# Optimization experiments

Measured on AMD Instinct MI355X. Metric: run time of the kernel, lower is better.

## Reference

```python
import jax, jax.numpy as jnp
import numpy as np

DIM = 1024
H = 16
DH = DIM // H  # 64


def _l2norm(a):
    # matches torch F.normalize(dim=-1, eps=1e-12)
    n = jnp.linalg.norm(a, axis=-1, keepdims=True)
    return a / jnp.maximum(n, 1e-12)


def setup_inputs() -> dict:
    key = jax.random.key(0)
    ks = jax.random.split(key, 6)
    B, T = 4, 4096
    s = 0.02
    return {
        "x": jax.random.normal(ks[0], (B, T, DIM), jnp.float32),
        "Wqkv": jax.random.normal(ks[1], (3 * DIM, DIM), jnp.float32) * s,
        "Wg": jax.random.normal(ks[2], (H, DIM), jnp.float32) * s,
        "bg": jnp.zeros((H,), jnp.float32),
        "Wb": jax.random.normal(ks[3], (H, DIM), jnp.float32) * s,
        "bb": jnp.zeros((H,), jnp.float32),
        "Wout": jax.random.normal(ks[4], (DIM, DIM), jnp.float32) * s,
    }


def reference(x, Wqkv, Wg, bg, Wb, bb, Wout):
    B, T, D = x.shape
    qkv = (x @ Wqkv.T).reshape(B, T, 3, H, DH)
    q = _l2norm(qkv[:, :, 0])   # [B,T,H,Dh]
    k = _l2norm(qkv[:, :, 1])
    v = qkv[:, :, 2]
    alpha = jax.nn.sigmoid(x @ Wg.T + bg)  # [B,T,H]
    beta = jax.nn.sigmoid(x @ Wb.T + bb)   # [B,T,H]

    # time-major for scan
    qT = jnp.moveaxis(q, 1, 0)  # [T,B,H,Dh]
    kT = jnp.moveaxis(k, 1, 0)
    vT = jnp.moveaxis(v, 1, 0)
    aT = jnp.moveaxis(alpha, 1, 0)  # [T,B,H]
    bT = jnp.moveaxis(beta, 1, 0)

    S0 = jnp.zeros((B, H, DH, DH), jnp.float32)

    def step(S, inp):
        q_t, k_t, v_t, a_t, b_t = inp
        Sk = jnp.einsum('bhij,bhj->bhi', S, k_t)          # S @ k_t
        a = a_t[..., None, None]
        b = b_t[..., None, None]
        # S = a * (S - b * (S k) k^T) + b * v k^T
        S = a * (S - b * Sk[..., :, None] * k_t[..., None, :]) \
            + b * v_t[..., :, None] * k_t[..., None, :]
        o = jnp.einsum('bhij,bhj->bhi', S, q_t)
        return S, o

    _, outs = jax.lax.scan(step, S0, (qT, kT, vT, aT, bT))  # [T,B,H,Dh]
    out = jnp.moveaxis(outs, 0, 1).reshape(B, T, D)
    return out @ Wout.T
```

## Files before the change

### kernel.cpp

```cpp
#include <hip/hip_runtime.h>
#include <hip/hip_bf16.h>

#define NB   4
#define NT   4096
#define BT   16384
#define NDIM 1024
#define NH   16
#define NDH  64
#define CC   64
#define NCH  (NT / CC)
#define NPAIR 64
#define NU   (NPAIR * NCH)
#define DBS  24

using u16 = unsigned short;
typedef __bf16 bf16x8 __attribute__((ext_vector_type(8)));
typedef float f32x4 __attribute__((ext_vector_type(4)));
typedef unsigned short u16x8 __attribute__((ext_vector_type(8)));
typedef unsigned short u16x4 __attribute__((ext_vector_type(4)));

__device__ __forceinline__ float bf2f(u16 b) { return __uint_as_float(((unsigned)b) << 16); }
__device__ __forceinline__ u16 f2bf(float f) {
  return __builtin_bit_cast(u16, __float2bfloat16(f));
}
__device__ __forceinline__ int swz(int row, int e) { return e ^ ((row & 7) << 3); }
__device__ __forceinline__ bf16x8 zfrag() {
  u16x8 z = {0, 0, 0, 0, 0, 0, 0, 0};
  return __builtin_bit_cast(bf16x8, z);
}

__global__ __launch_bounds__(256) void k_f32_to_bf16(const float* __restrict__ in,
                                                     u16* __restrict__ out, long n4) {
  long i = (long)blockIdx.x * blockDim.x + threadIdx.x;
  if (i >= n4) return;
  float4 f = reinterpret_cast<const float4*>(in)[i];
  u16x4 o;
  o.x = f2bf(f.x); o.y = f2bf(f.y); o.z = f2bf(f.z); o.w = f2bf(f.w);
  reinterpret_cast<u16x4*>(out)[i] = o;
}

__global__ __launch_bounds__(256) void k_build_wgb(const float* __restrict__ Wg,
                                                   const float* __restrict__ Wb,
                                                   u16* __restrict__ out) {
  int i = blockIdx.x * 256 + threadIdx.x;
  int row = i >> 10, col = i & 1023;
  float f = 0.f;
  if (row < 16)       f = Wg[row * 1024 + col];
  else if (row < 32)  f = Wb[(row - 16) * 1024 + col];
  out[i] = f2bf(f);
}

typedef unsigned int u32_as1 __attribute__((address_space(1)));
typedef unsigned int u32_as3 __attribute__((address_space(3)));
__device__ __forceinline__ void gload_lds16(const void* g, void* l) {
  __builtin_amdgcn_global_load_lds((const u32_as1*)g, (u32_as3*)l, 16, 0, 0);
}

template <typename OutT>
__global__ __launch_bounds__(256) void k_gemm_bt(const u16* __restrict__ A,
                                                 const u16* __restrict__ B,
                                                 OutT* __restrict__ C,
                                                 int M, int N, int K) {
  constexpr int BM = 128, BN = 128, BK = 32;
  __shared__ __align__(16) u16 As[BM * BK];
  __shared__ __align__(16) u16 Bs[BN * BK];
  const int tid = threadIdx.x;
  const int l = tid & 63, w = tid >> 6;
  const int tn = blockIdx.x, tm = blockIdx.y;
  const long a0 = (long)tm * BM * K;
  const long b0 = (long)tn * BN * K;
  const int srow = tid >> 2;
  const int scol = (tid & 3) << 3;
  const int wrow = (w >> 1) << 6;
  const int wcol = (w & 1) << 6;
  const int fr = l & 15, fq = l >> 4;

  f32x4 acc[4][4];
#pragma unroll
  for (int m = 0; m < 4; ++m)
#pragma unroll
    for (int n = 0; n < 4; ++n) acc[m][n] = f32x4{0.f, 0.f, 0.f, 0.f};

  for (int kk = 0; kk < K; kk += BK) {
    __syncthreads();
    const u16* gA = A + a0 + (long)srow * K + kk + scol;
    const u16* gB = B + b0 + (long)srow * K + kk + scol;
    gload_lds16(gA,                &As[(w * 16) * BK]);
    gload_lds16(gA + 64 * (long)K, &As[(64 + w * 16) * BK]);
    gload_lds16(gB,                &Bs[(w * 16) * BK]);
    gload_lds16(gB + 64 * (long)K, &Bs[(64 + w * 16) * BK]);
    __syncthreads();

    bf16x8 af[4], bfv[4];
#pragma unroll
    for (int m = 0; m < 4; ++m)
      af[m] = *(const bf16x8*)&As[(wrow + m * 16 + fr) * BK + (fq << 3)];
#pragma unroll
    for (int n = 0; n < 4; ++n)
      bfv[n] = *(const bf16x8*)&Bs[(wcol + n * 16 + fr) * BK + (fq << 3)];
#pragma unroll
    for (int m = 0; m < 4; ++m)
#pragma unroll
      for (int n = 0; n < 4; ++n)
        acc[m][n] = __builtin_amdgcn_mfma_f32_16x16x32_bf16(af[m], bfv[n], acc[m][n], 0, 0, 0);
  }

#pragma unroll
  for (int m = 0; m < 4; ++m) {
#pragma unroll
    for (int n = 0; n < 4; ++n) {
      const int r0 = tm * BM + wrow + m * 16 + fq * 4;
      const int c  = tn * BN + wcol + n * 16 + fr;
#pragma unroll
      for (int r = 0; r < 4; ++r) {
        float v = acc[m][n][r];
        long idx = (long)(r0 + r) * N + c;
        if constexpr (sizeof(OutT) == 2) C[idx] = f2bf(v);
        else                             C[idx] = v;
      }
    }
  }
}

template <typename OutT>
__global__ __launch_bounds__(512, 2) void k_gemm256(const u16* __restrict__ A,
                                                    const u16* __restrict__ B,
                                                    OutT* __restrict__ C,
                                                    int M, int N, int K) {
  __shared__ __align__(16) u16 As[2][2][256 * 32];
  __shared__ __align__(16) u16 Bs[2][2][256 * 32];
  const int tid = threadIdx.x;
  const int l = tid & 63, w = tid >> 6;
  const int wm = w >> 2, wn = w & 3;
  const int fr = l & 15, fq = l >> 4;
  const int nwg = gridDim.x;
  const int cpx = nwg >> 3;
  const int bid = blockIdx.x;
  const int sbid = (bid & 7) * cpx + (bid >> 3);
  const int ntn = N >> 8;
  const int tm = sbid / ntn, tn = sbid - tm * ntn;
  const long a0 = (long)tm * 256 * K;
  const long b0 = (long)tn * 256 * K;
  const int srow0 = tid >> 2;
  const int scol8 = (((tid & 3) ^ ((tid >> 4) & 3)) << 3);
  const int cswz = ((fq ^ ((fr >> 2) & 3)) << 3);
  const int NKT = K >> 6;

  auto stage_half = [&](int kt, int buf, int hf) {
    const int ks = hf >> 1;
    const u16* Gp = (hf & 1) ? B : A;
    const long g0 = ((hf & 1) ? b0 : a0) + (long)kt * 64 + ks * 32 + scol8;
    u16* lb = (hf & 1) ? &Bs[buf][ks][w * 512] : &As[buf][ks][w * 512];
#pragma unroll
    for (int r = 0; r < 2; ++r)
      gload_lds16(Gp + g0 + (long)(r * 128 + srow0) * K, lb + r * 4096);
  };

  f32x4 acc[8][4];
#pragma unroll
  for (int m = 0; m < 8; ++m)
#pragma unroll
    for (int n = 0; n < 4; ++n) acc[m][n] = f32x4{0.f, 0.f, 0.f, 0.f};

  stage_half(0, 0, 0); stage_half(0, 0, 1); stage_half(0, 0, 2); stage_half(0, 0, 3);

  for (int kt = 0; kt < NKT; ++kt) {
    const int bi = kt & 1;
    const bool pf = (kt + 1 < NKT);
    asm volatile("s_waitcnt vmcnt(4)" ::: "memory");
    __builtin_amdgcn_sched_barrier(0);
    __builtin_amdgcn_s_barrier();
    __builtin_amdgcn_sched_barrier(0);
    {
      const u16* ap = &As[bi][0][(wm * 128 + fr) * 32 + cswz];
      const u16* bp = &Bs[bi][0][(wn * 64 + fr) * 32 + cswz];
      bf16x8 bfr[4], afr[4];
#pragma unroll
      for (int n = 0; n < 4; ++n) bfr[n] = *(const bf16x8*)(bp + n * 512);
#pragma unroll
      for (int m = 0; m < 4; ++m) afr[m] = *(const bf16x8*)(ap + m * 512);
      if (pf) stage_half(kt + 1, bi ^ 1, 0);
      __builtin_amdgcn_s_setprio(1);
#pragma unroll
      for (int m = 0; m < 4; ++m)
#pragma unroll
        for (int n = 0; n < 4; ++n)
          acc[m][n] = __builtin_amdgcn_mfma_f32_16x16x32_bf16(afr[m], bfr[n], acc[m][n], 0, 0, 0);
      __builtin_amdgcn_s_setprio(0);
#pragma unroll
      for (int m = 0; m < 4; ++m) afr[m] = *(const bf16x8*)(ap + (4 + m) * 512);
      if (pf) stage_half(kt + 1, bi ^ 1, 1);
      __builtin_amdgcn_s_setprio(1);
#pragma unroll
      for (int m = 0; m < 4; ++m)
#pragma unroll
        for (int n = 0; n < 4; ++n)
          acc[4 + m][n] = __builtin_amdgcn_mfma_f32_16x16x32_bf16(afr[m], bfr[n], acc[4 + m][n], 0, 0, 0);
      __builtin_amdgcn_s_setprio(0);
    }
    if (pf) { asm volatile("s_waitcnt vmcnt(4)" ::: "memory"); }
    else    { asm volatile("s_waitcnt vmcnt(0)" ::: "memory"); }
    __builtin_amdgcn_sched_barrier(0);
    __builtin_amdgcn_s_barrier();
    __builtin_amdgcn_sched_barrier(0);
    {
      const u16* ap = &As[bi][1][(wm * 128 + fr) * 32 + cswz];
      const u16* bp = &Bs[bi][1][(wn * 64 + fr) * 32 + cswz];
      bf16x8 bfr[4], afr[4];
#pragma unroll
      for (int n = 0; n < 4; ++n) bfr[n] = *(const bf16x8*)(bp + n * 512);
#pragma unroll
      for (int m = 0; m < 4; ++m) afr[m] = *(const bf16x8*)(ap + m * 512);
      if (pf) stage_half(kt + 1, bi ^ 1, 2);
      __builtin_amdgcn_s_setprio(1);
#pragma unroll
      for (int m = 0; m < 4; ++m)
#pragma unroll
        for (int n = 0; n < 4; ++n)
          acc[m][n] = __builtin_amdgcn_mfma_f32_16x16x32_bf16(afr[m], bfr[n], acc[m][n], 0, 0, 0);
      __builtin_amdgcn_s_setprio(0);
#pragma unroll
      for (int m = 0; m < 4; ++m) afr[m] = *(const bf16x8*)(ap + (4 + m) * 512);
      if (pf) stage_half(kt + 1, bi ^ 1, 3);
      __builtin_amdgcn_s_setprio(1);
#pragma unroll
      for (int m = 0; m < 4; ++m)
#pragma unroll
        for (int n = 0; n < 4; ++n)
          acc[4 + m][n] = __builtin_amdgcn_mfma_f32_16x16x32_bf16(afr[m], bfr[n], acc[4 + m][n], 0, 0, 0);
      __builtin_amdgcn_s_setprio(0);
    }
  }

#pragma unroll
  for (int m = 0; m < 8; ++m)
#pragma unroll
    for (int n = 0; n < 4; ++n) {
      const int row0 = tm * 256 + wm * 128 + m * 16 + fq * 4;
      const int col  = tn * 256 + wn * 64 + n * 16 + fr;
#pragma unroll
      for (int r = 0; r < 4; ++r) {
        long idx = (long)(row0 + r) * N + col;
        if constexpr (sizeof(OutT) == 2) C[idx] = f2bf(acc[m][n][r]);
        else                             C[idx] = acc[m][n][r];
      }
    }
}

__global__ __launch_bounds__(256) void k_gates_fin(const float* __restrict__ raw,
                                                   const float* __restrict__ bg,
                                                   const float* __restrict__ bb,
                                                   float* __restrict__ alpha,
                                                   float* __restrict__ beta) {
  int i = blockIdx.x * 256 + threadIdx.x;
  if (i >= BT * NH) return;
  int bt = i >> 4, h = i & 15;
  float ga = raw[(long)bt * 128 + h] + bg[h];
  float gb = raw[(long)bt * 128 + 16 + h] + bb[h];
  alpha[i] = 1.f / (1.f + __expf(-ga));
  beta[i]  = 1.f / (1.f + __expf(-gb));
}

__global__ __launch_bounds__(256, 3) void k_prep(u16* __restrict__ qkv,
                                                 const float* __restrict__ alpha,
                                                 const float* __restrict__ beta,
                                                 float* __restrict__ A63G,
                                                 u16* __restrict__ ob) {
  __shared__ __align__(16) u16 Ks[64 * 64];
  __shared__ __align__(16) u16 WTs[128 * 64];
  __shared__ __align__(16) u16 Lb[64 * 64];
  __shared__ __align__(16) u16 MqS[64 * 64];
  __shared__ __align__(16) u16 KdT[64 * 64];
  __shared__ __align__(16) u16 Db[4 * 16 * DBS];
  __shared__ float cvec[64], Avec[64], bvec[64], nkinv[64], nqinv[64];

  const int unit = blockIdx.x;
  const int pair = unit >> 6, ch = unit & 63;
  const int b = pair >> 4, h = pair & 15;
  const int tid = threadIdx.x, l = tid & 63, w = tid >> 6;
  const int fr = l & 15, fq = l >> 4;
  const long t0 = (long)b * NT + (long)ch * CC;

  u16x8 kreg[2], vreg[2], qreg[2];
  int srow_[2], sseg_[2];
#pragma unroll
  for (int p = 0; p < 2; ++p) {
    int idx = p * 256 + tid;
    srow_[p] = idx >> 3; sseg_[p] = (idx & 7) * 8;
    long g = (t0 + srow_[p]) * 3072 + h * 64 + sseg_[p];
    qreg[p] = *(const u16x8*)&qkv[g];
    kreg[p] = *(const u16x8*)&qkv[g + 1024];
    vreg[p] = *(const u16x8*)&qkv[g + 2048];
  }
  const int ar = w * 16 + fr;
  u16x8 qa[2];
#pragma unroll
  for (int kk = 0; kk < 2; ++kk)
    qa[kk] = *(const u16x8*)&qkv[(t0 + ar) * 3072 + h * 64 + kk * 32 + fq * 8];

  if (tid < 64) { nkinv[tid] = 0.f; nqinv[tid] = 0.f; }
  if (w == 0) {
    float av = alpha[(t0 + l) * 16 + h];
    float bv = beta[(t0 + l) * 16 + h];
    float cl = __log2f(av);
#pragma unroll
    for (int d = 1; d < 64; d <<= 1) {
      float up = __shfl_up(cl, d);
      if (l >= d) cl += up;
    }
    float A = exp2f(cl);
    cvec[l] = cl; Avec[l] = A; bvec[l] = bv;
    if (l == 63) A63G[unit] = A;
  }
  __syncthreads();

#pragma unroll
  for (int p = 0; p < 2; ++p) {
    int row = srow_[p], seg = sseg_[p];
    *(u16x8*)&Ks[row * 64 + swz(row, seg)] = kreg[p];
    float kss = 0.f, qss = 0.f;
    const float bs = bvec[row];
#pragma unroll
    for (int e = 0; e < 8; ++e) {
      float kf = bf2f(kreg[p][e]), qf = bf2f(qreg[p][e]);
      kss += kf * kf; qss += qf * qf;
      int c = seg + e;
      WTs[c * 64 + swz(c, row)] = f2bf(bs * bf2f(vreg[p][e]));
    }
    atomicAdd(&nkinv[row], kss);
    atomicAdd(&nqinv[row], qss);
  }
  __syncthreads();

  if (tid < 64)       nkinv[tid] = rsqrtf(fmaxf(nkinv[tid], 1e-24f));
  else if (tid < 128) nqinv[tid - 64] = rsqrtf(fmaxf(nqinv[tid - 64], 1e-24f));
  __syncthreads();

  f32x4 akk[4], aqk[4];
#pragma unroll
  for (int n = 0; n < 4; ++n) { akk[n] = f32x4{0, 0, 0, 0}; aqk[n] = f32x4{0, 0, 0, 0}; }
  {
    bf16x8 afK[2], afQ[2];
#pragma unroll
    for (int kk = 0; kk < 2; ++kk) {
      afK[kk] = __builtin_bit_cast(bf16x8, *(const u16x8*)&Ks[ar * 64 + swz(ar, kk * 32 + fq * 8)]);
      afQ[kk] = __builtin_bit_cast(bf16x8, qa[kk]);
    }
#pragma unroll
    for (int n = 0; n < 4; ++n) {
      const int br = n * 16 + fr;
#pragma unroll
      for (int kk = 0; kk < 2; ++kk) {
        bf16x8 bk = __builtin_bit_cast(bf16x8, *(const u16x8*)&Ks[br * 64 + swz(br, kk * 32 + fq * 8)]);
        akk[n] = __builtin_amdgcn_mfma_f32_16x16x32_bf16(afK[kk], bk, akk[n], 0, 0, 0);
        aqk[n] = __builtin_amdgcn_mfma_f32_16x16x32_bf16(afQ[kk], bk, aqk[n], 0, 0, 0);
      }
    }
  }
  {
    const int j = tid & 63, tg4 = tid >> 6;
    const float c63 = cvec[63];
    u16 kb[16], kd[16];
#pragma unroll
    for (int tt = 0; tt < 16; ++tt) {
      int t = tg4 * 16 + tt;
      float kv = bf2f(Ks[t * 64 + swz(t, j)]) * nkinv[t];
      kb[tt] = f2bf(bvec[t] * Avec[t] * kv);
      kd[tt] = f2bf(exp2f(c63 - cvec[t]) * kv);
    }
#pragma unroll
    for (int g8 = 0; g8 < 2; ++g8) {
      u16x8 o1, o2;
#pragma unroll
      for (int e = 0; e < 8; ++e) { o1[e] = kb[g8 * 8 + e]; o2[e] = kd[g8 * 8 + e]; }
      int colg = tg4 * 16 + g8 * 8;
      *(u16x8*)&WTs[(64 + j) * 64 + swz(64 + j, colg)] = o1;
      *(u16x8*)&KdT[j * 64 + swz(j, colg)] = o2;
    }
  }
#pragma unroll
  for (int n = 0; n < 4; ++n)
#pragma unroll
    for (int r = 0; r < 4; ++r) {
      const int t = w * 16 + fq * 4 + r;
      const int s = n * 16 + fr;
      const float e = exp2f(cvec[t] - cvec[s]);
      Lb[t * 64 + swz(t, s)] = (s < t) ? f2bf(bvec[t] * e * nkinv[t] * nkinv[s] * akk[n][r]) : (u16)0;
      MqS[t * 64 + swz(t, s)] = (s <= t) ? f2bf(e * nqinv[t] * nkinv[s] * aqk[n][r]) : (u16)0;
    }
  __syncthreads();

  if (w == 0) {
    const int bi = l >> 4, c = l & 15;
    const int rb = bi * 16;
    float x[16];
#pragma unroll
    for (int u = 0; u < 16; ++u) {
      float a2 = (u == c) ? 1.f : 0.f;
#pragma unroll
      for (int s = 0; s < u; ++s)
        a2 -= bf2f(Lb[(rb + u) * 64 + swz(rb + u, rb + s)]) * x[s];
      x[u] = a2;
    }
#pragma unroll
    for (int u = 0; u < 16; ++u)
      Db[bi * 16 * DBS + u * DBS + c] = f2bf(x[u]);
  }
  __syncthreads();

  float ltil[6];
  {
    const int pbi[6] = {1, 2, 2, 3, 3, 3}, pbj[6] = {0, 0, 1, 0, 1, 2};
    const int tt = tid >> 4, s = tid & 15;
#pragma unroll
    for (int e = 0; e < 6; ++e) {
      int bi = pbi[e], bj = pbj[e];
      float a2 = 0.f;
#pragma unroll
      for (int u = 0; u < 16; ++u)
        a2 += bf2f(Db[bi * 16 * DBS + tt * DBS + u]) *
              bf2f(Lb[(bi * 16 + u) * 64 + swz(bi * 16 + u, bj * 16 + s)]);
      ltil[e] = a2;
    }
  }
  f32x4 rtacc[2][4];
#pragma unroll
  for (int rt2 = 0; rt2 < 2; ++rt2) {
    const int rrow = (w * 2 + rt2) * 16 + fr;
#pragma unroll
    for (int bi = 0; bi < 4; ++bi) {
      bf16x8 a2 = (fq < 2)
        ? __builtin_bit_cast(bf16x8, *(const u16x8*)&WTs[rrow * 64 + swz(rrow, bi * 16 + fq * 8)])
        : zfrag();
      bf16x8 b2 = (fq < 2)
        ? __builtin_bit_cast(bf16x8, *(const u16x8*)&Db[bi * 16 * DBS + fr * DBS + fq * 8])
        : zfrag();
      rtacc[rt2][bi] = __builtin_amdgcn_mfma_f32_16x16x32_bf16(a2, b2, f32x4{0, 0, 0, 0}, 0, 0, 0);
    }
  }
  __syncthreads();
  {
    const int pbi[6] = {1, 2, 2, 3, 3, 3}, pbj[6] = {0, 0, 1, 0, 1, 2};
    const int tt = tid >> 4, s = tid & 15;
#pragma unroll
    for (int e = 0; e < 6; ++e)
      Lb[(pbi[e] * 16 + tt) * 64 + swz(pbi[e] * 16 + tt, pbj[e] * 16 + s)] = f2bf(-ltil[e]);
  }
#pragma unroll
  for (int rt2 = 0; rt2 < 2; ++rt2)
#pragma unroll
    for (int bi = 0; bi < 4; ++bi)
#pragma unroll
      for (int r = 0; r < 4; ++r) {
        int rr = (w * 2 + rt2) * 16 + fq * 4 + r;
        WTs[rr * 64 + swz(rr, bi * 16 + fr)] = f2bf(rtacc[rt2][bi][r]);
      }
  __syncthreads();

#pragma unroll
  for (int rt2 = 0; rt2 < 2; ++rt2) {
    const int rrow = (w * 2 + rt2) * 16 + fr;
    const int wr0 = (w * 2 + rt2) * 16 + fq * 4;
#pragma unroll
    for (int i = 1; i < 4; ++i) {
      f32x4 a2;
#pragma unroll
      for (int r = 0; r < 4; ++r)
        a2[r] = bf2f(WTs[(wr0 + r) * 64 + swz(wr0 + r, i * 16 + fr)]);
      {
        bf16x8 af = __builtin_bit_cast(bf16x8, *(const u16x8*)&WTs[rrow * 64 + swz(rrow, fq * 8)]);
        bf16x8 bf_;
        if (i == 1) bf_ = (fq < 2)
          ? __builtin_bit_cast(bf16x8, *(const u16x8*)&Lb[(16 + fr) * 64 + swz(16 + fr, fq * 8)])
          : zfrag();
        else bf_ = __builtin_bit_cast(bf16x8, *(const u16x8*)&Lb[(i * 16 + fr) * 64 + swz(i * 16 + fr, fq * 8)]);
        a2 = __builtin_amdgcn_mfma_f32_16x16x32_bf16(af, bf_, a2, 0, 0, 0);
      }
      if (i == 3) {
        bf16x8 af = __builtin_bit_cast(bf16x8, *(const u16x8*)&WTs[rrow * 64 + swz(rrow, 32 + fq * 8)]);
        bf16x8 bf_ = (fq < 2)
          ? __builtin_bit_cast(bf16x8, *(const u16x8*)&Lb[(48 + fr) * 64 + swz(48 + fr, 32 + fq * 8)])
          : zfrag();
        a2 = __builtin_amdgcn_mfma_f32_16x16x32_bf16(af, bf_, a2, 0, 0, 0);
      }
#pragma unroll
      for (int r = 0; r < 4; ++r)
        WTs[(wr0 + r) * 64 + swz(wr0 + r, i * 16 + fr)] = f2bf(a2[r]);
    }
  }
  __syncthreads();

  u16 qpre[4][4];
#pragma unroll
  for (int n = 0; n < 4; ++n)
#pragma unroll
    for (int r = 0; r < 4; ++r)
      qpre[n][r] = qkv[(t0 + w * 16 + fq * 4 + r) * 3072 + h * 64 + n * 16 + fr];

  f32x4 aG[4], aU[4], aQe[4], aOi[4];
#pragma unroll
  for (int n = 0; n < 4; ++n) {
    aG[n] = f32x4{0, 0, 0, 0}; aU[n] = f32x4{0, 0, 0, 0};
    aQe[n] = f32x4{0, 0, 0, 0}; aOi[n] = f32x4{0, 0, 0, 0};
  }
  {
    bf16x8 aKd[2], aWv[2], aMq[2];
#pragma unroll
    for (int kk = 0; kk < 2; ++kk) {
      aKd[kk] = __builtin_bit_cast(bf16x8, *(const u16x8*)&KdT[ar * 64 + swz(ar, kk * 32 + fq * 8)]);
      aWv[kk] = __builtin_bit_cast(bf16x8, *(const u16x8*)&WTs[ar * 64 + swz(ar, kk * 32 + fq * 8)]);
      aMq[kk] = __builtin_bit_cast(bf16x8, *(const u16x8*)&MqS[ar * 64 + swz(ar, kk * 32 + fq * 8)]);
    }
#pragma unroll
    for (int n = 0; n < 4; ++n) {
      const int br = n * 16 + fr;
#pragma unroll
      for (int kk = 0; kk < 2; ++kk) {
        bf16x8 bTw = __builtin_bit_cast(bf16x8, *(const u16x8*)&WTs[(64 + br) * 64 + swz(64 + br, kk * 32 + fq * 8)]);
        bf16x8 bKd = __builtin_bit_cast(bf16x8, *(const u16x8*)&KdT[br * 64 + swz(br, kk * 32 + fq * 8)]);
        bf16x8 bWv = __builtin_bit_cast(bf16x8, *(const u16x8*)&WTs[br * 64 + swz(br, kk * 32 + fq * 8)]);
        aG[n]  = __builtin_amdgcn_mfma_f32_16x16x32_bf16(aKd[kk], bTw, aG[n], 0, 0, 0);
        aU[n]  = __builtin_amdgcn_mfma_f32_16x16x32_bf16(aWv[kk], bKd, aU[n], 0, 0, 0);
        aQe[n] = __builtin_amdgcn_mfma_f32_16x16x32_bf16(aMq[kk], bTw, aQe[n], 0, 0, 0);
        aOi[n] = __builtin_amdgcn_mfma_f32_16x16x32_bf16(aMq[kk], bWv, aOi[n], 0, 0, 0);
      }
    }
  }
  asm volatile("s_waitcnt vmcnt(0)" ::: "memory");
  __builtin_amdgcn_sched_barrier(0);
#pragma unroll
  for (int n = 0; n < 4; ++n)
#pragma unroll
    for (int r = 0; r < 4; ++r) {
      const int i = w * 16 + fq * 4 + r;
      const int cn = n * 16 + fr;
      const long grow = (t0 + i) * 3072 + h * 64 + swz(i, cn);
      qkv[grow]        = f2bf(Avec[i] * nqinv[i] * bf2f(qpre[n][r]) - aQe[n][r]);
      qkv[grow + 1024] = f2bf(-aG[n][r]);
      qkv[grow + 2048] = f2bf(aU[n][r]);
      ob[(t0 + i) * 1024 + h * 64 + cn] = f2bf(aOi[n][r]);
    }
}

__global__ __launch_bounds__(256) void k_seq(const u16* __restrict__ qkv,
                                             const float* __restrict__ A63G,
                                             u16* __restrict__ ob) {
  __shared__ __align__(16) u16 Sb[64 * 64];
  __shared__ __align__(16) u16 stg[2][4][64 * 64];
  __shared__ float a63s[64];
  const int pair = blockIdx.x;
  const int b = pair >> 4, h = pair & 15;
  const int tid = threadIdx.x, l = tid & 63, w = tid >> 6;
  const int fr = l & 15, fq = l >> 4;
  const int ar = w * 16 + fr;

  auto stage = [&](int c, int bi) {
    const long tg = (long)b * NT + (long)c * CC;
#pragma unroll
    for (int m = 0; m < 4; ++m)
#pragma unroll
      for (int p = 0; p < 2; ++p) {
        int idx = p * 256 + tid;
        int row = idx >> 3, seg = (idx & 7) * 8;
        const u16* src = (m < 3)
          ? &qkv[(tg + row) * 3072 + m * 1024 + h * 64 + seg]
          : &ob[(tg + row) * 1024 + h * 64 + seg];
        gload_lds16(src, &stg[bi][m][p * 2048 + w * 512]);
      }
  };

  if (tid < 64) a63s[tid] = A63G[pair * 64 + tid];
  for (int i = tid; i < 4096; i += 256) Sb[i] = 0;
  stage(0, 0);
  f32x4 sacc[4];
#pragma unroll
  for (int n = 0; n < 4; ++n) sacc[n] = f32x4{0, 0, 0, 0};
  asm volatile("s_waitcnt lgkmcnt(0)" ::: "memory");
  __builtin_amdgcn_sched_barrier(0);

  for (int c = 0; c < NCH; ++c) {
    const int bi = c & 1;
    const long tg = (long)b * NT + (long)c * CC;
    if (c + 1 < NCH) {
      stage(c + 1, bi ^ 1);
      asm volatile("s_waitcnt vmcnt(8)" ::: "memory");
    } else {
      asm volatile("s_waitcnt vmcnt(0)" ::: "memory");
    }
    __builtin_amdgcn_sched_barrier(0);
    __builtin_amdgcn_s_barrier();
    __builtin_amdgcn_sched_barrier(0);

    const u16* Qe = stg[bi][0];
    const u16* Gm = stg[bi][1];
    const u16* Um = stg[bi][2];
    const u16* Obl = stg[bi][3];

    bf16x8 aq[2];
#pragma unroll
    for (int kk = 0; kk < 2; ++kk)
      aq[kk] = __builtin_bit_cast(bf16x8, *(const u16x8*)&Qe[ar * 64 + swz(ar, kk * 32 + fq * 8)]);
    f32x4 ao[4];
#pragma unroll
    for (int n = 0; n < 4; ++n) ao[n] = f32x4{0, 0, 0, 0};
#pragma unroll
    for (int n = 0; n < 4; ++n) {
      const int br = n * 16 + fr;
#pragma unroll
      for (int kk = 0; kk < 2; ++kk) {
        bf16x8 sb = __builtin_bit_cast(bf16x8, *(const u16x8*)&Sb[br * 64 + swz(br, kk * 32 + fq * 8)]);
        ao[n] = __builtin_amdgcn_mfma_f32_16x16x32_bf16(aq[kk], sb, ao[n], 0, 0, 0);
      }
    }
    bf16x8 as_[2];
#pragma unroll
    for (int kk = 0; kk < 2; ++kk)
      as_[kk] = __builtin_bit_cast(bf16x8, *(const u16x8*)&Sb[ar * 64 + swz(ar, kk * 32 + fq * 8)]);
    const float A63 = a63s[c];
#pragma unroll
    for (int n = 0; n < 4; ++n) {
#pragma unroll
      for (int r = 0; r < 4; ++r) sacc[n][r] *= A63;
      const int br = n * 16 + fr;
#pragma unroll
      for (int kk = 0; kk < 2; ++kk) {
        bf16x8 g = __builtin_bit_cast(bf16x8, *(const u16x8*)&Gm[br * 64 + swz(br, kk * 32 + fq * 8)]);
        sacc[n] = __builtin_amdgcn_mfma_f32_16x16x32_bf16(as_[kk], g, sacc[n], 0, 0, 0);
      }
    }
#pragma unroll
    for (int n = 0; n < 4; ++n)
#pragma unroll
      for (int r = 0; r < 4; ++r) {
        const int i = w * 16 + fq * 4 + r;
        const int cn = n * 16 + fr;
        sacc[n][r] += bf2f(Um[i * 64 + swz(i, cn)]);
        float o = bf2f(Obl[i * 64 + cn]) + ao[n][r];
        ob[(tg + i) * 1024 + h * 64 + cn] = f2bf(o);
      }
    __builtin_amdgcn_s_barrier();
#pragma unroll
    for (int n = 0; n < 4; ++n)
#pragma unroll
      for (int r = 0; r < 4; ++r) {
        const int d = w * 16 + fq * 4 + r, j = n * 16 + fr;
        Sb[d * 64 + swz(d, j)] = f2bf(sacc[n][r]);
      }
    asm volatile("s_waitcnt lgkmcnt(0)" ::: "memory");
    __builtin_amdgcn_sched_barrier(0);
  }
}

extern "C" void kernel_launch(void* const* d_in, const int* in_sizes, int n_in,
                              void* d_out, int out_size, void* d_ws, size_t ws_size,
                              hipStream_t stream) {
  const float* x    = (const float*)d_in[0];
  const float* Wqkv = (const float*)d_in[1];
  const float* Wg   = (const float*)d_in[2];
  const float* bg   = (const float*)d_in[3];
  const float* Wb   = (const float*)d_in[4];
  const float* bb   = (const float*)d_in[5];
  const float* Wout = (const float*)d_in[6];
  float* out = (float*)d_out;

  char* ws = (char*)d_ws;
  u16* xb    = (u16*)ws;
  u16* wqkvb = xb    + (long)BT * NDIM;
  u16* woutb = wqkvb + (long)3072 * 1024;
  u16* wgbb  = woutb + (long)1024 * 1024;
  u16* qkvb  = wgbb  + (long)128 * 1024;
  u16* ob    = qkvb  + (long)BT * 3072;
  float* graw  = (float*)(ob + (long)BT * NDIM);
  float* alpha = graw + (long)BT * 128;
  float* beta  = alpha + (long)BT * NH;
  float* A63G  = graw;

  k_f32_to_bf16<<<(BT * (long)NDIM / 4 + 255) / 256, 256, 0, stream>>>(x, xb, BT * (long)NDIM / 4);
  k_f32_to_bf16<<<(3072L * 1024 / 4 + 255) / 256, 256, 0, stream>>>(Wqkv, wqkvb, 3072L * 1024 / 4);
  k_f32_to_bf16<<<(1024L * 1024 / 4 + 255) / 256, 256, 0, stream>>>(Wout, woutb, 1024L * 1024 / 4);
  k_build_wgb<<<(128 * 1024) / 256, 256, 0, stream>>>(Wg, Wb, wgbb);

  k_gemm256<u16><<<64 * 12, 512, 0, stream>>>(xb, wqkvb, qkvb, BT, 3072, NDIM);

  k_gemm_bt<float><<<dim3(1, BT / 128), 256, 0, stream>>>(xb, wgbb, graw, BT, 128, NDIM);
  k_gates_fin<<<(BT * NH + 255) / 256, 256, 0, stream>>>(graw, bg, bb, alpha, beta);

  k_prep<<<NU, 256, 0, stream>>>(qkvb, alpha, beta, A63G, ob);
  k_seq<<<NPAIR, 256, 0, stream>>>(qkvb, A63G, ob);

  k_gemm256<float><<<64 * 4, 512, 0, stream>>>(ob, woutb, out, BT, NDIM, NDIM);
}
```

Baseline: 443.8 us.

## Coalesce chunk outputs via LDS staging, replace atomics with shuffles, parallelize block solves

Per-chunk results of the prep kernel and the sequential kernel's outputs were written to global memory one scalar bf16 at a time. They are now staged in shared memory and written back as 16-byte vector stores. Row-norm accumulation switches from LDS atomicAdd to a warp shuffle reduction. The four 16x16 triangular solves now run on four wavefronts instead of one. The cost is extra barriers and an extra LDS buffer in k_seq, which may reduce occupancy or add latency to the serial loop.

```diff
diff --git a/kernel.cpp b/kernel.cpp
--- a/kernel.cpp
+++ b/kernel.cpp
@@ -298,7 +298,6 @@
   for (int kk = 0; kk < 2; ++kk)
     qa[kk] = *(const u16x8*)&qkv[(t0 + ar) * 3072 + h * 64 + kk * 32 + fq * 8];
 
-  if (tid < 64) { nkinv[tid] = 0.f; nqinv[tid] = 0.f; }
   if (w == 0) {
     float av = alpha[(t0 + l) * 16 + h];
     float bv = beta[(t0 + l) * 16 + h];
@@ -327,8 +326,9 @@
       int c = seg + e;
       WTs[c * 64 + swz(c, row)] = f2bf(bs * bf2f(vreg[p][e]));
     }
-    atomicAdd(&nkinv[row], kss);
-    atomicAdd(&nqinv[row], qss);
+    kss += __shfl_xor(kss, 1); kss += __shfl_xor(kss, 2); kss += __shfl_xor(kss, 4);
+    qss += __shfl_xor(qss, 1); qss += __shfl_xor(qss, 2); qss += __shfl_xor(qss, 4);
+    if ((tid & 7) == 0) { nkinv[row] = kss; nqinv[row] = qss; }
   }
   __syncthreads();
 
@@ -390,9 +390,9 @@
     }
   __syncthreads();
 
-  if (w == 0) {
-    const int bi = l >> 4, c = l & 15;
-    const int rb = bi * 16;
+  if (l < 16) {
+    const int c = l;
+    const int rb = w * 16;
     float x[16];
 #pragma unroll
     for (int u = 0; u < 16; ++u) {
@@ -404,7 +404,7 @@
     }
 #pragma unroll
     for (int u = 0; u < 16; ++u)
-      Db[bi * 16 * DBS + u * DBS + c] = f2bf(x[u]);
+      Db[w * 16 * DBS + u * DBS + c] = f2bf(x[u]);
   }
   __syncthreads();
 
@@ -527,25 +527,37 @@
     }
   }
   asm volatile("s_waitcnt vmcnt(0)" ::: "memory");
-  __builtin_amdgcn_sched_barrier(0);
+  __syncthreads();
 #pragma unroll
   for (int n = 0; n < 4; ++n)
 #pragma unroll
     for (int r = 0; r < 4; ++r) {
       const int i = w * 16 + fq * 4 + r;
       const int cn = n * 16 + fr;
-      const long grow = (t0 + i) * 3072 + h * 64 + swz(i, cn);
-      qkv[grow]        = f2bf(Avec[i] * nqinv[i] * bf2f(qpre[n][r]) - aQe[n][r]);
-      qkv[grow + 1024] = f2bf(-aG[n][r]);
-      qkv[grow + 2048] = f2bf(aU[n][r]);
-      ob[(t0 + i) * 1024 + h * 64 + cn] = f2bf(aOi[n][r]);
-    }
+      const int sw = i * 64 + swz(i, cn);
+      Ks[sw]  = f2bf(Avec[i] * nqinv[i] * bf2f(qpre[n][r]) - aQe[n][r]);
+      Lb[sw]  = f2bf(-aG[n][r]);
+      MqS[sw] = f2bf(aU[n][r]);
+      KdT[i * 64 + cn] = f2bf(aOi[n][r]);
+    }
+  __syncthreads();
+#pragma unroll
+  for (int p = 0; p < 2; ++p) {
+    const int idx = p * 256 + tid;
+    const int row = idx >> 3, seg = (idx & 7) * 8;
+    const long gr = (t0 + row) * 3072 + h * 64 + seg;
+    *(u16x8*)&qkv[gr]        = *(const u16x8*)&Ks[row * 64 + seg];
+    *(u16x8*)&qkv[gr + 1024] = *(const u16x8*)&Lb[row * 64 + seg];
+    *(u16x8*)&qkv[gr + 2048] = *(const u16x8*)&MqS[row * 64 + seg];
+    *(u16x8*)&ob[(t0 + row) * 1024 + h * 64 + seg] = *(const u16x8*)&KdT[row * 64 + seg];
+  }
 }
 
 __global__ __launch_bounds__(256) void k_seq(const u16* __restrict__ qkv,
                                              const float* __restrict__ A63G,
                                              u16* __restrict__ ob) {
   __shared__ __align__(16) u16 Sb[64 * 64];
+  __shared__ __align__(16) u16 Obs[64 * 64];
   __shared__ __align__(16) u16 stg[2][4][64 * 64];
   __shared__ float a63s[64];
   const int pair = blockIdx.x;
@@ -635,9 +647,9 @@
         const int i = w * 16 + fq * 4 + r;
         const int cn = n * 16 + fr;
         sacc[n][r] += bf2f(Um[i * 64 + swz(i, cn)]);
-        float o = bf2f(Obl[i * 64 + cn]) + ao[n][r];
-        ob[(tg + i) * 1024 + h * 64 + cn] = f2bf(o);
-      }
+        Obs[i * 64 + cn] = f2bf(bf2f(Obl[i * 64 + cn]) + ao[n][r]);
+      }
+    asm volatile("s_waitcnt lgkmcnt(0)" ::: "memory");
     __builtin_amdgcn_s_barrier();
 #pragma unroll
     for (int n = 0; n < 4; ++n)
@@ -646,6 +658,12 @@
         const int d = w * 16 + fq * 4 + r, j = n * 16 + fr;
         Sb[d * 64 + swz(d, j)] = f2bf(sacc[n][r]);
       }
+#pragma unroll
+    for (int p = 0; p < 2; ++p) {
+      const int idx = p * 256 + tid;
+      const int row = idx >> 3, seg = (idx & 7) * 8;
+      *(u16x8*)&ob[(tg + row) * 1024 + h * 64 + seg] = *(const u16x8*)&Obs[row * 64 + seg];
+    }
     asm volatile("s_waitcnt lgkmcnt(0)" ::: "memory");
     __builtin_amdgcn_sched_barrier(0);
   }
```

Result: slower. 469.8 us (+5.9%).
